# Kernel tuning notes

Hardware: AMD Instinct MI355X
Metric: run time of the kernel (lower is better)

## Reference

```python
import jax, jax.numpy as jnp
import numpy as np

C = 512
NUM_GROUPS = 32
EPS = 1e-6


def setup_inputs() -> dict:
    key = jax.random.key(0)
    ks = jax.random.split(key, 6)
    B, H, W = 4, 64, 64
    x = jax.random.normal(ks[0], (B, H, W, C), dtype=jnp.float32)
    # GroupNorm affine params (flax default init: scale=1, bias=0)
    gn_scale = jnp.ones((C,), jnp.float32)
    gn_bias = jnp.zeros((C,), jnp.float32)
    # 1x1 convs == per-pixel dense layers; weight [C_in, C_out], bias [C_out]
    def dense(k):
        return jax.random.normal(k, (C, C), dtype=jnp.float32) * 0.02
    wq, wk, wv, wo = dense(ks[1]), dense(ks[2]), dense(ks[3]), dense(ks[4])
    bq = jnp.zeros((C,), jnp.float32)
    bk = jnp.zeros((C,), jnp.float32)
    bv = jnp.zeros((C,), jnp.float32)
    bo = jnp.zeros((C,), jnp.float32)
    return {"x": x, "gn_scale": gn_scale, "gn_bias": gn_bias,
            "wq": wq, "bq": bq, "wk": wk, "bk": bk,
            "wv": wv, "bv": bv, "wo": wo, "bo": bo}


def _group_norm(x, scale, bias):
    B, H, W, Cc = x.shape
    g = NUM_GROUPS
    xg = x.reshape(B, H, W, g, Cc // g)
    mean = jnp.mean(xg, axis=(1, 2, 4), keepdims=True)
    var = jnp.var(xg, axis=(1, 2, 4), keepdims=True)
    xn = (xg - mean) * jax.lax.rsqrt(var + EPS)
    xn = xn.reshape(B, H, W, Cc)
    return xn * scale + bias


def reference(x, gn_scale, gn_bias, wq, bq, wk, bk, wv, bv, wo, bo):
    B, H, W, Cc = x.shape
    hn = _group_norm(x, gn_scale, gn_bias)
    # 1x1 convs
    q = (hn @ wq + bq).reshape(B, H * W, Cc)
    k = (hn @ wk + bk).reshape(B, H * W, Cc)
    v = (hn @ wv + bv).reshape(B, H * W, Cc)
    scale = jnp.asarray(Cc, x.dtype) ** -0.5
    # scores[b,i,j] = <q_i, k_j> * c^-0.5; softmax over keys j
    attn = jax.nn.softmax(jnp.einsum('bic,bjc->bij', q, k) * scale, axis=-1)
    out = jnp.einsum('bij,bjc->bic', attn, v).reshape(B, H, W, Cc)
    return x + (out @ wo + bo)
```

## Files before the change

kernel.cpp:

```cpp
#include <hip/hip_runtime.h>


typedef __attribute__((ext_vector_type(8))) __bf16 bf16x8;
typedef __attribute__((ext_vector_type(4))) __bf16 bf16x4;
typedef __attribute__((ext_vector_type(4))) float  floatx4;

#define C_DIM 512
#define SPB   4096
#define MTOT  16384

#define HN_OFF  ((size_t)0)
#define Q_OFF   ((size_t)16 << 20)
#define K_OFF   ((size_t)32 << 20)
#define V4_OFF  ((size_t)48 << 20)
#define WT_OFF  ((size_t)64 << 20)
#define O1_OFF  ((size_t)68 << 20)
#define ML_OFF  ((size_t)84 << 20)
#define GS_OFF  (ML_OFF + (size_t)(256 << 10))

__device__ inline floatx4 mfma16(bf16x8 a, bf16x8 b, floatx4 c) {
    return __builtin_amdgcn_mfma_f32_16x16x32_bf16(a, b, c, 0, 0, 0);
}

__device__ inline void gload16(const void* g, void* lds) {
    __builtin_amdgcn_global_load_lds(
        (const __attribute__((address_space(1))) unsigned int*)g,
        (__attribute__((address_space(3))) unsigned int*)lds, 16, 0, 0);
}

__global__ __launch_bounds__(256) void zero_stats(float* gstats) {
    gstats[threadIdx.x] = 0.f;
}

__global__ __launch_bounds__(256) void gn_stats(
    const float* __restrict__ x, float* __restrict__ gstats) {
    int bg = blockIdx.x;
    int b = bg >> 5, g = bg & 31;
    int tid = threadIdx.x;
    int cq = tid & 3, s0 = tid >> 2;
    const float* base = x + (size_t)b * SPB * C_DIM + g * 16 + cq * 4
                          + (size_t)blockIdx.y * 1024 * C_DIM;
    float sum = 0.f, sq = 0.f;
#pragma unroll 4
    for (int i = 0; i < 16; ++i) {
        floatx4 v = *(const floatx4*)(base + (size_t)(i * 64 + s0) * C_DIM);
        sum += v[0] + v[1] + v[2] + v[3];
        sq  += v[0]*v[0] + v[1]*v[1] + v[2]*v[2] + v[3]*v[3];
    }
#pragma unroll
    for (int off = 1; off < 64; off <<= 1) {
        sum += __shfl_xor(sum, off);
        sq  += __shfl_xor(sq,  off);
    }
    __shared__ float sm[8];
    int w = tid >> 6, lane = tid & 63;
    if (lane == 0) { sm[w] = sum; sm[4 + w] = sq; }
    __syncthreads();
    if (tid == 0) {
        atomicAdd(&gstats[bg * 2],     sm[0] + sm[1] + sm[2] + sm[3]);
        atomicAdd(&gstats[bg * 2 + 1], sm[4] + sm[5] + sm[6] + sm[7]);
    }
}

__global__ __launch_bounds__(256) void gn_apply(
    const float* __restrict__ x, const float* __restrict__ gstats,
    const float* __restrict__ gsc, const float* __restrict__ gbi,
    __bf16* __restrict__ hn) {
    int bg = blockIdx.x;
    int b = bg >> 5, g = bg & 31;
    int tid = threadIdx.x;
    int cq = tid & 3, s0 = tid >> 2;
    float S  = gstats[bg * 2], Qs = gstats[bg * 2 + 1];
    float mean = S * (1.f / 65536.f);
    float var  = Qs * (1.f / 65536.f) - mean * mean;
    float rstd = rsqrtf(var + 1e-6f);
    float sc[4], bi[4];
#pragma unroll
    for (int j = 0; j < 4; ++j) {
        float s_ = gsc[g * 16 + cq * 4 + j] * rstd;
        sc[j] = s_;
        bi[j] = gbi[g * 16 + cq * 4 + j] - mean * s_;
    }
    size_t off = (size_t)b * SPB * C_DIM + g * 16 + cq * 4
               + (size_t)blockIdx.y * 1024 * C_DIM;
    const float* base = x + off;
    __bf16* hbase = hn + off;
#pragma unroll 4
    for (int i = 0; i < 16; ++i) {
        floatx4 v = *(const floatx4*)(base + (size_t)(i * 64 + s0) * C_DIM);
        bf16x4 o;
#pragma unroll
        for (int j = 0; j < 4; ++j) o[j] = (__bf16)(v[j] * sc[j] + bi[j]);
        *(bf16x4*)(hbase + (size_t)(i * 64 + s0) * C_DIM) = o;
    }
}

__global__ __launch_bounds__(256) void wt_kernel(
    const float* __restrict__ w0, const float* __restrict__ w1,
    const float* __restrict__ w2, const float* __restrict__ w3,
    __bf16* __restrict__ wt) {
    const float* srcs[4] = {w0, w1, w2, w3};
    const float* src = srcs[blockIdx.z];
    __bf16* dst = wt + (size_t)blockIdx.z * C_DIM * C_DIM;
    __shared__ float tile[32][33];
    int tx = threadIdx.x & 31, ty = threadIdx.x >> 5;
    int gx = blockIdx.x * 32, gy = blockIdx.y * 32;
#pragma unroll
    for (int i = 0; i < 4; ++i)
        tile[ty + i * 8][tx] = src[(size_t)(gy + ty + i * 8) * C_DIM + gx + tx];
    __syncthreads();
#pragma unroll
    for (int i = 0; i < 4; ++i) {
        int n = gx + ty + i * 8;
        int k = gy + tx;
        dst[(size_t)n * C_DIM + k] = (__bf16)tile[tx][ty + i * 8];
    }
}

__global__ __launch_bounds__(256, 2) void proj_qkv(
    const __bf16* __restrict__ hn, const __bf16* __restrict__ wt_all,
    const float* __restrict__ bq, const float* __restrict__ bk,
    const float* __restrict__ bv, __bf16* __restrict__ qout,
    __bf16* __restrict__ kout, __bf16* __restrict__ v4out) {
    int z = blockIdx.z;
    const __bf16* wt = wt_all + (size_t)z * C_DIM * C_DIM;
    const float* bias = (z == 0) ? bq : (z == 1) ? bk : bv;
    __shared__ __bf16 Alds[128 * 32];
    __shared__ __bf16 Blds[128 * 32];
    int tid = threadIdx.x, lane = tid & 63, w = tid >> 6;
    int c = lane & 15, quad = lane >> 4;
    int wm = w & 1, wn = w >> 1;
    int mbase = blockIdx.x * 128, nbase = blockIdx.y * 128;
    floatx4 acc[4][4] = {};
    for (int kb = 0; kb < 16; ++kb) {
        __syncthreads();
#pragma unroll
        for (int p = 0; p < 2; ++p) {
            int chunk0 = w * 128 + p * 64;
            int chunk = chunk0 + lane;
            int row = chunk >> 2, qk = chunk & 3;
            gload16(hn + (size_t)(mbase + row) * C_DIM + kb * 32 + qk * 8, Alds + chunk0 * 8);
            gload16(wt + (size_t)(nbase + row) * C_DIM + kb * 32 + qk * 8, Blds + chunk0 * 8);
        }
        __syncthreads();
        bf16x8 af[4], bfr[4];
#pragma unroll
        for (int mt = 0; mt < 4; ++mt)
            af[mt] = *(const bf16x8*)(Alds + (wm * 64 + mt * 16 + c) * 32 + quad * 8);
#pragma unroll
        for (int nt = 0; nt < 4; ++nt)
            bfr[nt] = *(const bf16x8*)(Blds + (wn * 64 + nt * 16 + c) * 32 + quad * 8);
#pragma unroll
        for (int mt = 0; mt < 4; ++mt)
#pragma unroll
            for (int nt = 0; nt < 4; ++nt)
                acc[mt][nt] = mfma16(af[mt], bfr[nt], acc[mt][nt]);
    }
    float scale = (z == 0) ? 0.0441941738241592f : 1.0f;
#pragma unroll
    for (int nt = 0; nt < 4; ++nt) {
        int n = nbase + wn * 64 + nt * 16 + c;
        float bval = bias[n];
#pragma unroll
        for (int mt = 0; mt < 4; ++mt) {
            int m0 = mbase + wm * 64 + mt * 16 + quad * 4;
#pragma unroll
            for (int r = 0; r < 4; ++r) {
                int m = m0 + r;
                float val = (acc[mt][nt][r] + bval) * scale;
                if (z == 0)      qout[(size_t)m * C_DIM + n] = (__bf16)val;
                else if (z == 1) kout[(size_t)m * C_DIM + n] = (__bf16)val;
                else {
                    int bb = m >> 12, pos = m & 4095;
                    v4out[((size_t)(bb * 512 + (pos >> 3)) * C_DIM + n) * 8 + (pos & 7)] = (__bf16)val;
                }
            }
        }
    }
}

__device__ inline void stage_K(const __bf16* kbase, int key0,
                               __bf16* Klds, int w, int lane) {
#pragma unroll
    for (int p = 0; p < 8; ++p) {
        int chunk0 = w * 512 + p * 64;
        int chunk = chunk0 + lane;
        gload16(kbase + (size_t)(key0 + (chunk & 31)) * C_DIM + (chunk >> 5) * 8,
                Klds + chunk0 * 8);
    }
}

__device__ inline void stage_V(const __bf16* vsrc, __bf16* Vlds, int w, int lane) {
#pragma unroll
    for (int p = 0; p < 8; ++p) {
        int chunk0 = w * 512 + p * 64;
        gload16(vsrc + (size_t)(chunk0 + lane) * 8, Vlds + chunk0 * 8);
    }
}

__global__ __launch_bounds__(256, 2) void flash_kernel(
    const __bf16* __restrict__ q, const __bf16* __restrict__ kmat,
    const __bf16* __restrict__ v4, __bf16* __restrict__ op0,
    __bf16* __restrict__ op1, float* __restrict__ lpart) {
    __shared__ __bf16 Klds[16384];
    __shared__ __bf16 Vlds[16384];
    __shared__ __bf16 Plds[64 * 40];
    int tid = threadIdx.x, lane = tid & 63, w = tid >> 6;
    int c = lane & 15, quad = lane >> 4;
    int bid = blockIdx.x;
    int h = bid & 1, qt = (bid >> 1) & 63, b = bid >> 7;

    const __bf16* qp = q + ((size_t)(b * SPB + qt * 64 + w * 16 + c)) * C_DIM + quad * 8;
    bf16x8 qf[16];
#pragma unroll
    for (int ks = 0; ks < 16; ++ks) qf[ks] = *(const bf16x8*)(qp + ks * 32);
    floatx4 o[4][8];
#pragma unroll
    for (int mg = 0; mg < 4; ++mg)
#pragma unroll
        for (int t = 0; t < 8; ++t) o[mg][t] = (floatx4){0.f, 0.f, 0.f, 0.f};
    float l_r[4] = {0.f, 0.f, 0.f, 0.f};

    const __bf16* kbase = kmat + (size_t)b * SPB * C_DIM;
    const __bf16* vbase = v4 + (size_t)b * 512 * C_DIM * 8;

    stage_K(kbase, h * 2048, Klds, w, lane);
    __syncthreads();

    for (int kt = 0; kt < 64; ++kt) {
        int key0 = h * 2048 + kt * 32;
        stage_V(vbase + (size_t)(key0 >> 3) * C_DIM * 8, Vlds, w, lane);
        floatx4 s0 = (floatx4){0.f,0.f,0.f,0.f}, s1 = (floatx4){0.f,0.f,0.f,0.f};
#pragma unroll
        for (int ks = 0; ks < 16; ++ks) {
            bf16x8 k0 = *(const bf16x8*)(Klds + (((ks * 4 + quad) * 32) + c) * 8);
            bf16x8 k1 = *(const bf16x8*)(Klds + (((ks * 4 + quad) * 32) + c + 16) * 8);
            s0 = mfma16(qf[ks], k0, s0);
            s1 = mfma16(qf[ks], k1, s1);
        }
#pragma unroll
        for (int r = 0; r < 4; ++r) {
            float p0 = __expf(s0[r]);
            float p1 = __expf(s1[r]);
            l_r[r] += p0 + p1;
            int row = w * 16 + quad * 4 + r;
            Plds[row * 40 + c]      = (__bf16)p0;
            Plds[row * 40 + c + 16] = (__bf16)p1;
        }
        __syncthreads();
        int kn = (kt < 63) ? kt + 1 : 63;
        stage_K(kbase, h * 2048 + kn * 32, Klds, w, lane);
        bf16x8 pf[4];
#pragma unroll
        for (int mg = 0; mg < 4; ++mg)
            pf[mg] = *(const bf16x8*)(Plds + (mg * 16 + c) * 40 + quad * 8);
#pragma unroll
        for (int t = 0; t < 8; ++t) {
            bf16x8 vf = *(const bf16x8*)(Vlds + ((size_t)quad * 512 + w * 128 + t * 16 + c) * 8);
#pragma unroll
            for (int mg = 0; mg < 4; ++mg)
                o[mg][t] = mfma16(pf[mg], vf, o[mg][t]);
        }
        __syncthreads();
    }
#pragma unroll
    for (int r = 0; r < 4; ++r) {
        float l = l_r[r];
        l += __shfl_xor(l, 1);
        l += __shfl_xor(l, 2);
        l += __shfl_xor(l, 4);
        l += __shfl_xor(l, 8);
        l_r[r] = l;
    }
    if (c == 0) {
#pragma unroll
        for (int r = 0; r < 4; ++r) {
            int grow = b * SPB + qt * 64 + w * 16 + quad * 4 + r;
            lpart[h * MTOT + grow] = l_r[r];
        }
    }
    __bf16* ob = h ? op1 : op0;
#pragma unroll
    for (int mg = 0; mg < 4; ++mg)
#pragma unroll
        for (int t = 0; t < 8; ++t)
#pragma unroll
            for (int r = 0; r < 4; ++r) {
                int grow = b * SPB + qt * 64 + mg * 16 + quad * 4 + r;
                ob[(size_t)grow * C_DIM + w * 128 + t * 16 + c] = (__bf16)o[mg][t][r];
            }
}

__global__ __launch_bounds__(256) void combine_kernel(
    const __bf16* __restrict__ o0, const __bf16* __restrict__ o1,
    const float* __restrict__ lpart, __bf16* __restrict__ attn) {
    int tid = threadIdx.x, lane = tid & 63, w = tid >> 6;
    int rbase = blockIdx.x * 64 + w * 16;
    for (int rr = 0; rr < 16; ++rr) {
        int row = rbase + rr;
        float inv = 1.f / (lpart[row] + lpart[MTOT + row]);
        bf16x8 v0 = *(const bf16x8*)(o0 + (size_t)row * C_DIM + lane * 8);
        bf16x8 v1 = *(const bf16x8*)(o1 + (size_t)row * C_DIM + lane * 8);
        bf16x8 r;
#pragma unroll
        for (int j = 0; j < 8; ++j) r[j] = (__bf16)(((float)v0[j] + (float)v1[j]) * inv);
        *(bf16x8*)(attn + (size_t)row * C_DIM + lane * 8) = r;
    }
}

__global__ __launch_bounds__(256, 2) void proj_out(
    const __bf16* __restrict__ attn, const __bf16* __restrict__ wot,
    const float* __restrict__ bo, const float* __restrict__ x,
    float* __restrict__ out) {
    __shared__ __bf16 Alds[128 * 32];
    __shared__ __bf16 Blds[128 * 32];
    int tid = threadIdx.x, lane = tid & 63, w = tid >> 6;
    int c = lane & 15, quad = lane >> 4;
    int wm = w & 1, wn = w >> 1;
    int mbase = blockIdx.x * 128, nbase = blockIdx.y * 128;
    floatx4 acc[4][4] = {};
    for (int kb = 0; kb < 16; ++kb) {
        __syncthreads();
#pragma unroll
        for (int p = 0; p < 2; ++p) {
            int chunk0 = w * 128 + p * 64;
            int chunk = chunk0 + lane;
            int row = chunk >> 2, qk = chunk & 3;
            gload16(attn + (size_t)(mbase + row) * C_DIM + kb * 32 + qk * 8, Alds + chunk0 * 8);
            gload16(wot + (size_t)(nbase + row) * C_DIM + kb * 32 + qk * 8, Blds + chunk0 * 8);
        }
        __syncthreads();
        bf16x8 af[4], bfr[4];
#pragma unroll
        for (int mt = 0; mt < 4; ++mt)
            af[mt] = *(const bf16x8*)(Alds + (wm * 64 + mt * 16 + c) * 32 + quad * 8);
#pragma unroll
        for (int nt = 0; nt < 4; ++nt)
            bfr[nt] = *(const bf16x8*)(Blds + (wn * 64 + nt * 16 + c) * 32 + quad * 8);
#pragma unroll
        for (int mt = 0; mt < 4; ++mt)
#pragma unroll
            for (int nt = 0; nt < 4; ++nt)
                acc[mt][nt] = mfma16(af[mt], bfr[nt], acc[mt][nt]);
    }
#pragma unroll
    for (int nt = 0; nt < 4; ++nt) {
        int n = nbase + wn * 64 + nt * 16 + c;
        float bval = bo[n];
#pragma unroll
        for (int mt = 0; mt < 4; ++mt) {
            int m0 = mbase + wm * 64 + mt * 16 + quad * 4;
#pragma unroll
            for (int r = 0; r < 4; ++r) {
                size_t idx = (size_t)(m0 + r) * C_DIM + n;
                out[idx] = acc[mt][nt][r] + bval + x[idx];
            }
        }
    }
}

extern "C" void kernel_launch(void* const* d_in, const int* in_sizes, int n_in,
                              void* d_out, int out_size, void* d_ws, size_t ws_size,
                              hipStream_t stream) {
    const float* x   = (const float*)d_in[0];
    const float* gsc = (const float*)d_in[1];
    const float* gbi = (const float*)d_in[2];
    const float* wq  = (const float*)d_in[3];
    const float* bq  = (const float*)d_in[4];
    const float* wk  = (const float*)d_in[5];
    const float* bk  = (const float*)d_in[6];
    const float* wv  = (const float*)d_in[7];
    const float* bv  = (const float*)d_in[8];
    const float* wo  = (const float*)d_in[9];
    const float* bo  = (const float*)d_in[10];
    char* ws = (char*)d_ws;
    __bf16* hn  = (__bf16*)(ws + HN_OFF);
    __bf16* qb  = (__bf16*)(ws + Q_OFF);
    __bf16* kb  = (__bf16*)(ws + K_OFF);
    __bf16* v4  = (__bf16*)(ws + V4_OFF);
    __bf16* wt  = (__bf16*)(ws + WT_OFF);
    __bf16* op0 = (__bf16*)(ws + HN_OFF);
    __bf16* op1 = (__bf16*)(ws + O1_OFF);
    float*  lp  = (float*)(ws + ML_OFF);
    float*  gs  = (float*)(ws + GS_OFF);
    __bf16* attn = qb;
    float* out = (float*)d_out;

    zero_stats<<<1, 256, 0, stream>>>(gs);
    wt_kernel<<<dim3(16, 16, 4), 256, 0, stream>>>(wq, wk, wv, wo, wt);
    gn_stats<<<dim3(128, 4), 256, 0, stream>>>(x, gs);
    gn_apply<<<dim3(128, 4), 256, 0, stream>>>(x, gs, gsc, gbi, hn);
    proj_qkv<<<dim3(128, 4, 3), 256, 0, stream>>>(hn, wt, bq, bk, bv, qb, kb, v4);
    flash_kernel<<<512, 256, 0, stream>>>(qb, kb, v4, op0, op1, lp);
    combine_kernel<<<256, 256, 0, stream>>>(op0, op1, lp, attn);
    proj_out<<<dim3(128, 4), 256, 0, stream>>>(attn, wt + (size_t)3 * C_DIM * C_DIM, bo, x, out);
}
```

Before: 445.0 us.

## Restructure flash kernel with 32x32 MFMA, split-K scores and double-buffered K

Switches the attention inner loop from 16x16x32 to 32x32x16 bf16 MFMAs. Warps are split 2x2 over query rows and channel halves, so the QK^T partial sums are exchanged through LDS before the exponent. K tiles are now double-buffered in LDS, dropping one barrier per iteration. V fragments are loaded straight from global memory instead of being staged in LDS, and P goes through a swizzled LDS layout. This is meant to cut LDS traffic and barrier stalls and raise MFMA efficiency, at the cost of extra global-load latency for V and an added cross-warp reduction step.

```diff
diff --git a/kernel.cpp b/kernel.cpp
--- a/kernel.cpp
+++ b/kernel.cpp
@@ -4,6 +4,7 @@
 typedef __attribute__((ext_vector_type(8))) __bf16 bf16x8;
 typedef __attribute__((ext_vector_type(4))) __bf16 bf16x4;
 typedef __attribute__((ext_vector_type(4))) float  floatx4;
+typedef __attribute__((ext_vector_type(16))) float floatx16;
 
 #define C_DIM 512
 #define SPB   4096
@@ -20,6 +21,10 @@
 
 __device__ inline floatx4 mfma16(bf16x8 a, bf16x8 b, floatx4 c) {
     return __builtin_amdgcn_mfma_f32_16x16x32_bf16(a, b, c, 0, 0, 0);
+}
+
+__device__ inline floatx16 mfma32(bf16x8 a, bf16x8 b, floatx16 c) {
+    return __builtin_amdgcn_mfma_f32_32x32x16_bf16(a, b, c, 0, 0, 0);
 }
 
 __device__ inline void gload16(const void* g, void* lds) {
@@ -190,104 +195,136 @@
     }
 }
 
-__device__ inline void stage_V(const __bf16* vsrc, __bf16* Vlds, int w, int lane) {
-#pragma unroll
-    for (int p = 0; p < 8; ++p) {
-        int chunk0 = w * 512 + p * 64;
-        gload16(vsrc + (size_t)(chunk0 + lane) * 8, Vlds + chunk0 * 8);
-    }
-}
-
 __global__ __launch_bounds__(256, 2) void flash_kernel(
     const __bf16* __restrict__ q, const __bf16* __restrict__ kmat,
     const __bf16* __restrict__ v4, __bf16* __restrict__ op0,
     __bf16* __restrict__ op1, float* __restrict__ lpart) {
-    __shared__ __bf16 Klds[16384];
-    __shared__ __bf16 Vlds[16384];
-    __shared__ __bf16 Plds[64 * 40];
+    __shared__ __bf16 Klds[2][16384];
+    __shared__ float  Splds[4][64][8];
+    __shared__ __bf16 Plds[2048];
+
     int tid = threadIdx.x, lane = tid & 63, w = tid >> 6;
-    int c = lane & 15, quad = lane >> 4;
+    int l31 = lane & 31, h2 = lane >> 5;
+    int wr = w & 1, wc = w >> 1;
     int bid = blockIdx.x;
     int h = bid & 1, qt = (bid >> 1) & 63, b = bid >> 7;
 
-    const __bf16* qp = q + ((size_t)(b * SPB + qt * 64 + w * 16 + c)) * C_DIM + quad * 8;
+    const __bf16* qp = q + ((size_t)(b * SPB + qt * 64 + wr * 32 + l31)) * C_DIM
+                         + wc * 256 + h2 * 8;
     bf16x8 qf[16];
 #pragma unroll
-    for (int ks = 0; ks < 16; ++ks) qf[ks] = *(const bf16x8*)(qp + ks * 32);
-    floatx4 o[4][8];
-#pragma unroll
-    for (int mg = 0; mg < 4; ++mg)
-#pragma unroll
-        for (int t = 0; t < 8; ++t) o[mg][t] = (floatx4){0.f, 0.f, 0.f, 0.f};
-    float l_r[4] = {0.f, 0.f, 0.f, 0.f};
+    for (int kk = 0; kk < 16; ++kk) qf[kk] = *(const bf16x8*)(qp + kk * 16);
+
+    floatx16 o[2][4];
+#pragma unroll
+    for (int rt = 0; rt < 2; ++rt)
+#pragma unroll
+        for (int ct = 0; ct < 4; ++ct)
+#pragma unroll
+            for (int i = 0; i < 16; ++i) o[rt][ct][i] = 0.f;
+    float l_r[8] = {0.f, 0.f, 0.f, 0.f, 0.f, 0.f, 0.f, 0.f};
 
     const __bf16* kbase = kmat + (size_t)b * SPB * C_DIM;
     const __bf16* vbase = v4 + (size_t)b * 512 * C_DIM * 8;
 
-    stage_K(kbase, h * 2048, Klds, w, lane);
+    stage_K(kbase, h * 2048, &Klds[0][0], w, lane);
     __syncthreads();
-
+    int cur = 0;
     for (int kt = 0; kt < 64; ++kt) {
         int key0 = h * 2048 + kt * 32;
-        stage_V(vbase + (size_t)(key0 >> 3) * C_DIM * 8, Vlds, w, lane);
-        floatx4 s0 = (floatx4){0.f,0.f,0.f,0.f}, s1 = (floatx4){0.f,0.f,0.f,0.f};
-#pragma unroll
-        for (int ks = 0; ks < 16; ++ks) {
-            bf16x8 k0 = *(const bf16x8*)(Klds + (((ks * 4 + quad) * 32) + c) * 8);
-            bf16x8 k1 = *(const bf16x8*)(Klds + (((ks * 4 + quad) * 32) + c + 16) * 8);
-            s0 = mfma16(qf[ks], k0, s0);
-            s1 = mfma16(qf[ks], k1, s1);
-        }
-#pragma unroll
-        for (int r = 0; r < 4; ++r) {
-            float p0 = __expf(s0[r]);
-            float p1 = __expf(s1[r]);
-            l_r[r] += p0 + p1;
-            int row = w * 16 + quad * 4 + r;
-            Plds[row * 40 + c]      = (__bf16)p0;
-            Plds[row * 40 + c + 16] = (__bf16)p1;
-        }
-        __syncthreads();
         int kn = (kt < 63) ? kt + 1 : 63;
-        stage_K(kbase, h * 2048 + kn * 32, Klds, w, lane);
-        bf16x8 pf[4];
-#pragma unroll
-        for (int mg = 0; mg < 4; ++mg)
-            pf[mg] = *(const bf16x8*)(Plds + (mg * 16 + c) * 40 + quad * 8);
-#pragma unroll
-        for (int t = 0; t < 8; ++t) {
-            bf16x8 vf = *(const bf16x8*)(Vlds + ((size_t)quad * 512 + w * 128 + t * 16 + c) * 8);
-#pragma unroll
-            for (int mg = 0; mg < 4; ++mg)
-                o[mg][t] = mfma16(pf[mg], vf, o[mg][t]);
-        }
-        __syncthreads();
-    }
-#pragma unroll
-    for (int r = 0; r < 4; ++r) {
-        float l = l_r[r];
+        stage_K(kbase, h * 2048 + kn * 32, &Klds[cur ^ 1][0], w, lane);
+        floatx16 s;
+#pragma unroll
+        for (int i = 0; i < 16; ++i) s[i] = 0.f;
+        const __bf16* Kb = &Klds[cur][0];
+#pragma unroll
+        for (int kk = 0; kk < 16; ++kk) {
+            bf16x8 kf = *(const bf16x8*)(Kb + ((wc * 32 + kk * 2 + h2) * 32 + l31) * 8);
+            s = mfma32(qf[kk], kf, s);
+        }
+        float* sp = &Splds[wr * 2 + wc][lane][0];
+        floatx4 w0, w1;
+        if (wc == 0) {
+            w0 = (floatx4){s[8],  s[9],  s[10], s[11]};
+            w1 = (floatx4){s[12], s[13], s[14], s[15]};
+        } else {
+            w0 = (floatx4){s[0], s[1], s[2], s[3]};
+            w1 = (floatx4){s[4], s[5], s[6], s[7]};
+        }
+        *(floatx4*)sp = w0;
+        *(floatx4*)(sp + 4) = w1;
+        __syncthreads();
+        const float* pp = &Splds[wr * 2 + (wc ^ 1)][lane][0];
+        floatx4 q0 = *(const floatx4*)pp;
+        floatx4 q1 = *(const floatx4*)(pp + 4);
+        float p8[8];
+        if (wc == 0) {
+            p8[0] = __expf(s[0] + q0[0]);  p8[1] = __expf(s[1] + q0[1]);
+            p8[2] = __expf(s[2] + q0[2]);  p8[3] = __expf(s[3] + q0[3]);
+            p8[4] = __expf(s[4] + q1[0]);  p8[5] = __expf(s[5] + q1[1]);
+            p8[6] = __expf(s[6] + q1[2]);  p8[7] = __expf(s[7] + q1[3]);
+        } else {
+            p8[0] = __expf(s[8]  + q0[0]); p8[1] = __expf(s[9]  + q0[1]);
+            p8[2] = __expf(s[10] + q0[2]); p8[3] = __expf(s[11] + q0[3]);
+            p8[4] = __expf(s[12] + q1[0]); p8[5] = __expf(s[13] + q1[1]);
+            p8[6] = __expf(s[14] + q1[2]); p8[7] = __expf(s[15] + q1[3]);
+        }
+        char* praw = (char*)Plds;
+#pragma unroll
+        for (int e = 0; e < 8; ++e) {
+            l_r[e] += p8[e];
+            int r = wc * 8 + e;
+            int row = (r & 3) + 8 * (r >> 2) + 4 * h2;
+            int off = (wr * 32 + row) * 64 + ((l31 * 2) ^ (((row >> 1) & 3) << 4));
+            *(__bf16*)(praw + off) = (__bf16)p8[e];
+        }
+        __syncthreads();
+#pragma unroll
+        for (int ks = 0; ks < 2; ++ks) {
+            int chunk = (ks * 2 + h2) ^ ((l31 >> 1) & 3);
+            bf16x8 pa0 = *(const bf16x8*)(praw + (l31) * 64 + (chunk << 4));
+            bf16x8 pa1 = *(const bf16x8*)(praw + (32 + l31) * 64 + (chunk << 4));
+            int pg = (key0 >> 3) + ks * 2 + h2;
+            const __bf16* vp = vbase + ((size_t)pg * C_DIM + w * 128 + l31) * 8;
+#pragma unroll
+            for (int ct = 0; ct < 4; ++ct) {
+                bf16x8 vf = *(const bf16x8*)(vp + ct * 32 * 8);
+                o[0][ct] = mfma32(pa0, vf, o[0][ct]);
+                o[1][ct] = mfma32(pa1, vf, o[1][ct]);
+            }
+        }
+        cur ^= 1;
+    }
+#pragma unroll
+    for (int e = 0; e < 8; ++e) {
+        float l = l_r[e];
         l += __shfl_xor(l, 1);
         l += __shfl_xor(l, 2);
         l += __shfl_xor(l, 4);
         l += __shfl_xor(l, 8);
-        l_r[r] = l;
-    }
-    if (c == 0) {
-#pragma unroll
-        for (int r = 0; r < 4; ++r) {
-            int grow = b * SPB + qt * 64 + w * 16 + quad * 4 + r;
-            lpart[h * MTOT + grow] = l_r[r];
+        l += __shfl_xor(l, 16);
+        l_r[e] = l;
+    }
+    if (l31 == 0) {
+#pragma unroll
+        for (int e = 0; e < 8; ++e) {
+            int r = wc * 8 + e;
+            int row = (r & 3) + 8 * (r >> 2) + 4 * h2;
+            int grow = b * SPB + qt * 64 + wr * 32 + row;
+            lpart[h * MTOT + grow] = l_r[e];
         }
     }
     __bf16* ob = h ? op1 : op0;
 #pragma unroll
-    for (int mg = 0; mg < 4; ++mg)
-#pragma unroll
-        for (int t = 0; t < 8; ++t)
-#pragma unroll
-            for (int r = 0; r < 4; ++r) {
-                int grow = b * SPB + qt * 64 + mg * 16 + quad * 4 + r;
-                ob[(size_t)grow * C_DIM + w * 128 + t * 16 + c] = (__bf16)o[mg][t][r];
+    for (int rt = 0; rt < 2; ++rt)
+#pragma unroll
+        for (int ct = 0; ct < 4; ++ct)
+#pragma unroll
+            for (int r = 0; r < 16; ++r) {
+                int row = (r & 3) + 8 * (r >> 2) + 4 * h2;
+                int grow = b * SPB + qt * 64 + rt * 32 + row;
+                ob[(size_t)grow * C_DIM + w * 128 + ct * 32 + l31] = (__bf16)o[rt][ct][r];
             }
 }
 
```

After: 706.4 us. 58.7% more time.
